# Optimization experiments

Measured on AMD Instinct MI355X. Metric: run time of the kernel, lower is better.

## Reference

```python
import jax, jax.numpy as jnp
import numpy as np

B, S, E, H, L, A, OBS = 4, 1024, 512, 8, 4, 8, 128
D_HEAD = E // H
EPS = 1e-6
DECAY_SCALING = 1.0


def rmsnorm(x, scale):
    return x * jax.lax.rsqrt(jnp.mean(x * x, -1, keepdims=True) + EPS) * scale


def swiglu_ffn(x, w_gate, w_lin, w_out):
    return (jax.nn.silu(x @ w_gate) * (x @ w_lin)) @ w_out


def retention(x, h, logk, w_q, w_k, w_v, w_g, w_o, gns, gnb, ts, seg):
    # x:[B,S,E]  h:[B,H,d,d]  ts/seg:[B,S] int  logk:[H]
    q = (x @ w_q).reshape(B, S, H, D_HEAD).transpose(0, 2, 1, 3)
    k = (x @ w_k).reshape(B, S, H, D_HEAD).transpose(0, 2, 1, 3) / jnp.sqrt(jnp.asarray(D_HEAD, x.dtype))
    v = (x @ w_v).reshape(B, S, H, D_HEAD).transpose(0, 2, 1, 3)
    dt = (ts[:, :, None] - ts[:, None, :]).astype(x.dtype)            # [B,S,S]
    mask = (dt >= 0) & (seg[:, :, None] == seg[:, None, :])           # timestep-causal, same episode
    dt = jnp.where(mask, dt, 0.0)
    Dm = jnp.where(mask[:, None], jnp.exp(dt[:, None] * logk[None, :, None, None]), 0.0)  # [B,H,S,S]
    scores = jnp.einsum('bhnd,bhmd->bhnm', q, k) * Dm
    inner = jnp.einsum('bhnm,bhme->bhne', scores, v)
    tsf = ts.astype(x.dtype)
    fresh = (seg == 0).astype(x.dtype)                                # prev-chunk state only valid pre-done
    xi = jnp.exp((tsf + 1.0)[:, None, :] * logk[None, :, None]) * fresh[:, None, :]  # [B,H,S]
    cross = jnp.einsum('bhn,bhnd,bhde->bhne', xi, q, h)
    ret = inner + cross                                               # [B,H,S,d]
    # chunk-final recurrent state
    tmax = tsf[:, -1]
    eta = jnp.exp((tmax[:, None] - tsf)[:, None, :] * logk[None, :, None])
    eta = eta * (seg == seg[:, -1:]).astype(x.dtype)[:, None, :]
    keep = (seg[:, -1] == 0).astype(x.dtype)
    h_decay = jnp.exp((tmax + 1.0)[:, None] * logk[None, :]) * keep[:, None]  # [B,H]
    h_new = h * h_decay[..., None, None] + jnp.einsum('bhm,bhmd,bhme->bhde', eta, k, v)
    # per-head group norm (num_groups = n_head)
    y = ret.transpose(0, 2, 1, 3)                                     # [B,S,H,d]
    mu = jnp.mean(y, -1, keepdims=True)
    var = jnp.mean((y - mu) ** 2, -1, keepdims=True)
    y = ((y - mu) * jax.lax.rsqrt(var + EPS)).reshape(B, S, E) * gns + gnb
    out = (jax.nn.silu(x @ w_g) * y) @ w_o
    return out, h_new


def forward(obs, hstate, dones, timestep_id, ln_enc_scale, w_enc, ln_shared,
            wq, wk, wv, wg, wo, gn_scale, gn_bias, ln1_s, ln2_s,
            sw_gate, sw_lin, sw_out, head_w1, head_b1, head_ln, head_w2, head_b2):
    kappas = (1.0 - jnp.exp(jnp.linspace(jnp.log(1.0 / 32.0), jnp.log(1.0 / 512.0), H))) * DECAY_SCALING
    logk = jnp.log(kappas).astype(obs.dtype)
    seg = jnp.cumsum(dones, axis=-1)
    x = jax.nn.gelu(rmsnorm(obs, ln_enc_scale) @ w_enc)               # obs encoder
    new_h = jnp.zeros_like(hstate)
    for i in range(L):
        xin = rmsnorm(x, ln_shared)
        ret, hn = retention(xin, hstate[:, :, i], logk, wq[i], wk[i], wv[i], wg[i], wo[i],
                            gn_scale[i], gn_bias[i], timestep_id, seg)
        x1 = rmsnorm(xin + ret, ln1_s[i])
        x = rmsnorm(x1 + swiglu_ffn(x1, sw_gate[i], sw_lin[i], sw_out[i]), ln2_s[i])
        new_h = new_h.at[:, :, i].set(hn)
    z = jax.nn.gelu(x @ head_w1 + head_b1)
    v_loc = rmsnorm(z, head_ln) @ head_w2 + head_b2
    return v_loc, x, new_h


def setup_inputs() -> dict:
    key = jax.random.key(0)
    ks = jax.random.split(key, 16)
    sc = 0.02
    f = jnp.float32
    return {
        'obs': jax.random.normal(ks[0], (B, S, OBS), f),
        'hstate': jax.random.normal(ks[1], (B, H, L, D_HEAD, D_HEAD), f) * 0.1,
        'dones': (jax.random.uniform(ks[2], (B, S)) < 0.01).astype(jnp.int32),
        'timestep_id': jnp.broadcast_to(jnp.repeat(jnp.arange(S // A, dtype=jnp.int32), A)[None], (B, S)),
        'ln_enc_scale': jnp.ones((OBS,), f),
        'w_enc': jax.random.normal(ks[3], (OBS, E), f) * sc,
        'ln_shared': jnp.ones((E,), f),
        'wq': jax.random.normal(ks[4], (L, E, E), f) * sc,
        'wk': jax.random.normal(ks[5], (L, E, E), f) * sc,
        'wv': jax.random.normal(ks[6], (L, E, E), f) * sc,
        'wg': jax.random.normal(ks[7], (L, E, E), f) * sc,
        'wo': jax.random.normal(ks[8], (L, E, E), f) * sc,
        'gn_scale': jnp.ones((L, E), f),
        'gn_bias': jnp.zeros((L, E), f),
        'ln1_s': jnp.ones((L, E), f),
        'ln2_s': jnp.ones((L, E), f),
        'sw_gate': jax.random.normal(ks[9], (L, E, E), f) * sc,
        'sw_lin': jax.random.normal(ks[10], (L, E, E), f) * sc,
        'sw_out': jax.random.normal(ks[11], (L, E, E), f) * sc,
        'head_w1': jax.random.normal(ks[12], (E, E), f) * sc,
        'head_b1': jnp.zeros((E,), f),
        'head_ln': jnp.ones((E,), f),
        'head_w2': jax.random.normal(ks[13], (E, 1), f) * 0.01,
        'head_b2': jnp.zeros((1,), f),
    }


def reference(obs, hstate, dones, timestep_id, ln_enc_scale, w_enc, ln_shared,
              wq, wk, wv, wg, wo, gn_scale, gn_bias, ln1_s, ln2_s,
              sw_gate, sw_lin, sw_out, head_w1, head_b1, head_ln, head_w2, head_b2):
    return forward(obs, hstate, dones, timestep_id, ln_enc_scale, w_enc, ln_shared,
                   wq, wk, wv, wg, wo, gn_scale, gn_bias, ln1_s, ln2_s,
                   sw_gate, sw_lin, sw_out, head_w1, head_b1, head_ln, head_w2, head_b2)
```

## Files before the change

### kernel.cpp

```cpp
#include <hip/hip_runtime.h>
#include <math.h>

#define BN 4
#define SN 1024
#define EN 512
#define HN 8
#define LN 4
#define DN 64
#define OBSN 128
#define NR (BN*SN)
#define NB (NR*EN)
#define EPSF 1e-6f

typedef __attribute__((ext_vector_type(8))) short short8v;
typedef __attribute__((ext_vector_type(4))) float f32x4;
typedef unsigned short u16;

__device__ __forceinline__ float logk_of(int h){
    const float start = -3.4657359027997265f;
    const float step  = -0.3960841031771117f;
    return logf(1.0f - expf(start + step*(float)h));
}
__device__ __forceinline__ float geluf(float x){
    float x3 = x*x*x;
    return 0.5f*x*(1.0f + tanhf(0.7978845608028654f*(x + 0.044715f*x3)));
}
__device__ __forceinline__ float siluf(float x){
    return x / (1.0f + expf(-x));
}
__device__ __forceinline__ u16 f2bf(float x){
    union { float f; unsigned u; } v; v.f = x;
    unsigned r = v.u + 0x7FFFu + ((v.u >> 16) & 1u);
    return (u16)(r >> 16);
}
__device__ __forceinline__ float bf2f(u16 x){
    union { unsigned u; float f; } v; v.u = ((unsigned)x)<<16;
    return v.f;
}
__device__ __forceinline__ void load_lds16(const void* g, void* l){
    __builtin_amdgcn_global_load_lds((const __attribute__((address_space(1))) void*)g,
                                     (__attribute__((address_space(3))) void*)l, 16, 0, 0);
}
__device__ __forceinline__ int swz(int r, int bo){ return r*128 + (bo ^ ((r&7)<<4)); }

__global__ void seg_kernel(const int* __restrict__ dones, int* __restrict__ seg){
    __shared__ int sm[SN];
    int b = blockIdx.x, t = threadIdx.x;
    sm[t] = dones[b*SN + t];
    __syncthreads();
    for (int off=1; off<SN; off<<=1){
        int v = (t>=off) ? sm[t-off] : 0;
        __syncthreads();
        sm[t] += v;
        __syncthreads();
    }
    seg[b*SN + t] = sm[t];
}

__global__ void wconv8_kernel(const float* w0, const float* w1, const float* w2,
                              const float* w3, const float* w4, const float* w5,
                              const float* w6, const float* w7,
                              u16* __restrict__ dst){
    __shared__ u16 tile[32][33];
    int z = blockIdx.z;
    int type = z>>2, layer = z&3;
    const float* srcs[8] = {w0,w1,w2,w3,w4,w5,w6,w7};
    const float* s = srcs[type] + (size_t)layer*EN*EN;
    u16* d = dst + ((size_t)type*LN + layer)*EN*EN;
    int k0 = blockIdx.y*32, m0 = blockIdx.x*32;
    int tx = threadIdx.x, ty = threadIdx.y;
    #pragma unroll
    for (int i=0;i<32;i+=8)
        tile[tx][ty+i] = f2bf(s[(size_t)(k0+ty+i)*EN + m0+tx]);
    __syncthreads();
    #pragma unroll
    for (int i=0;i<32;i+=8)
        d[(size_t)(m0+ty+i)*EN + k0+tx] = tile[ty+i][tx];
}
__global__ void wconv_kernel(const float* __restrict__ src, u16* __restrict__ dst,
                             int K, int M){
    __shared__ u16 tile[32][33];
    int k0 = blockIdx.y*32, m0 = blockIdx.x*32;
    int tx = threadIdx.x, ty = threadIdx.y;
    #pragma unroll
    for (int i=0;i<32;i+=8)
        tile[tx][ty+i] = f2bf(src[(size_t)(k0+ty+i)*M + m0+tx]);
    __syncthreads();
    #pragma unroll
    for (int i=0;i<32;i+=8)
        dst[(size_t)(m0+ty+i)*K + k0+tx] = tile[ty+i][tx];
}

template<int COLS, bool WF32, bool WBF>
__global__ void rmsnorm_kernel(const float* __restrict__ A,
                               const float* __restrict__ scale,
                               float* __restrict__ Of,
                               u16* __restrict__ Ob){
    constexpr int PER = COLS/64;
    int row  = blockIdx.x*4 + (threadIdx.x>>6);
    int lane = threadIdx.x & 63;
    const float* a = A + (size_t)row*COLS;
    float v[PER];
    float ss = 0.f;
    #pragma unroll
    for (int i=0;i<PER;i++){
        float x = a[lane + i*64];
        v[i] = x; ss += x*x;
    }
    #pragma unroll
    for (int off=32; off>0; off>>=1) ss += __shfl_xor(ss, off, 64);
    float rs = rsqrtf(ss*(1.0f/COLS) + EPSF);
    #pragma unroll
    for (int i=0;i<PER;i++){
        float o = v[i]*rs*scale[lane + i*64];
        if (WF32) Of[(size_t)row*COLS + lane + i*64] = o;
        if (WBF)  Ob[(size_t)row*COLS + lane + i*64] = f2bf(o);
    }
}

__device__ __forceinline__ void stage_tile(const u16* __restrict__ G, size_t rowBase,
                                           int K, int k0, u16* dst, int t){
    #pragma unroll
    for (int i=0;i<2;i++){
        int o = i*4096 + t*16;
        int grow = o>>7, gcolb = o&127;
        load_lds16(G + (rowBase+grow)*K + k0 + (gcolb>>1), (char*)dst + o);
    }
}
__device__ __forceinline__ void mma_tile(const u16* As, const u16* Bs, f32x4 acc[2][2],
                                         int wr, int wc, int lane){
    #pragma unroll
    for (int kk=0; kk<64; kk+=32){
        int kb = kk + (lane>>4)*8;
        short8v a[2], b[2];
        #pragma unroll
        for (int m=0;m<2;m++)
            a[m] = *(const short8v*)((const char*)As + (wr*32+m*16+(lane&15))*128 + kb*2);
        #pragma unroll
        for (int n=0;n<2;n++)
            b[n] = *(const short8v*)((const char*)Bs + (wc*32+n*16+(lane&15))*128 + kb*2);
        #pragma unroll
        for (int m=0;m<2;m++)
            #pragma unroll
            for (int n=0;n<2;n++)
                acc[m][n] = __builtin_amdgcn_mfma_f32_16x16x32_bf16(a[m], b[n], acc[m][n], 0,0,0);
    }
}
#define ZERO_ACC(acc) { _Pragma("unroll") for (int m=0;m<2;m++) _Pragma("unroll") for (int n=0;n<2;n++){ acc[m][n][0]=0.f;acc[m][n][1]=0.f;acc[m][n][2]=0.f;acc[m][n][3]=0.f; } }

__global__ __launch_bounds__(256) void gemm_qkvg(
    const u16* __restrict__ A,
    const u16* __restrict__ WQ, const u16* __restrict__ WK,
    const u16* __restrict__ WV, const u16* __restrict__ WG,
    u16* __restrict__ Qbb, u16* __restrict__ Kbb,
    u16* __restrict__ VtT, u16* __restrict__ KtT, float* __restrict__ Gb)
{
    __shared__ u16 As[2][64*64];
    __shared__ u16 Bs[2][4][64*64];
    int t = threadIdx.x;
    int row0 = blockIdx.y*64, col0 = blockIdx.x*64;
    int w = t>>6, lane = t&63;
    int wr = w>>1, wc = w&1;
    f32x4 accQ[2][2], accK[2][2], accV[2][2], accG[2][2];
    ZERO_ACC(accQ); ZERO_ACC(accK); ZERO_ACC(accV); ZERO_ACC(accG);
    const u16* Ws[4] = {WQ, WK, WV, WG};

    stage_tile(A, (size_t)row0, EN, 0, As[0], t);
    #pragma unroll
    for (int wt=0; wt<4; wt++) stage_tile(Ws[wt], (size_t)col0, EN, 0, Bs[0][wt], t);
    __syncthreads();
    for (int ti=0; ti<EN/64; ++ti){
        int cur = ti&1;
        if (ti+1 < EN/64){
            stage_tile(A, (size_t)row0, EN, (ti+1)*64, As[cur^1], t);
            #pragma unroll
            for (int wt=0; wt<4; wt++)
                stage_tile(Ws[wt], (size_t)col0, EN, (ti+1)*64, Bs[cur^1][wt], t);
        }
        mma_tile(As[cur], Bs[cur][0], accQ, wr, wc, lane);
        mma_tile(As[cur], Bs[cur][1], accK, wr, wc, lane);
        mma_tile(As[cur], Bs[cur][2], accV, wr, wc, lane);
        mma_tile(As[cur], Bs[cur][3], accG, wr, wc, lane);
        __syncthreads();
    }
    #pragma unroll
    for (int m=0;m<2;m++){
        #pragma unroll
        for (int n=0;n<2;n++){
            int col = col0 + wc*32 + n*16 + (lane&15);
            int rbase = row0 + wr*32 + m*16 + (lane>>4)*4;
            ushort4 pkV, pkK;
            #pragma unroll
            for (int j=0;j<4;j++){
                size_t idx = (size_t)(rbase+j)*EN + col;
                Qbb[idx] = f2bf(accQ[m][n][j]);
                float kx = accK[m][n][j]*0.125f;
                Kbb[idx] = f2bf(kx);
                ((u16*)&pkK)[j] = f2bf(kx);
                ((u16*)&pkV)[j] = f2bf(accV[m][n][j]);
                Gb[idx] = siluf(accG[m][n][j]);
            }
            int bb = rbase>>10;
            int s0 = rbase&1023;
            *(ushort4*)(VtT + ((size_t)bb*EN + col)*SN + s0) = pkV;
            *(ushort4*)(KtT + ((size_t)bb*EN + col)*SN + s0) = pkK;
        }
    }
}

__global__ __launch_bounds__(256) void gemm_swpair(
    const u16* __restrict__ A,
    const u16* __restrict__ WGt, const u16* __restrict__ WLt,
    u16* __restrict__ Out)
{
    __shared__ u16 As[2][64*64];
    __shared__ u16 Bg[2][64*64];
    __shared__ u16 Bl[2][64*64];
    int t = threadIdx.x;
    int row0 = blockIdx.y*64, col0 = blockIdx.x*64;
    int w = t>>6, lane = t&63;
    int wr = w>>1, wc = w&1;
    f32x4 accG[2][2], accL[2][2];
    ZERO_ACC(accG); ZERO_ACC(accL);
    stage_tile(A, (size_t)row0, EN, 0, As[0], t);
    stage_tile(WGt, (size_t)col0, EN, 0, Bg[0], t);
    stage_tile(WLt, (size_t)col0, EN, 0, Bl[0], t);
    __syncthreads();
    for (int ti=0; ti<EN/64; ++ti){
        int cur = ti&1;
        if (ti+1 < EN/64){
            stage_tile(A, (size_t)row0, EN, (ti+1)*64, As[cur^1], t);
            stage_tile(WGt, (size_t)col0, EN, (ti+1)*64, Bg[cur^1], t);
            stage_tile(WLt, (size_t)col0, EN, (ti+1)*64, Bl[cur^1], t);
        }
        mma_tile(As[cur], Bg[cur], accG, wr, wc, lane);
        mma_tile(As[cur], Bl[cur], accL, wr, wc, lane);
        __syncthreads();
    }
    #pragma unroll
    for (int m=0;m<2;m++){
        #pragma unroll
        for (int n=0;n<2;n++){
            int col = col0 + wc*32 + n*16 + (lane&15);
            int rbase = row0 + wr*32 + m*16 + (lane>>4)*4;
            #pragma unroll
            for (int j=0;j<4;j++){
                float x = siluf(accG[m][n][j]) * accL[m][n][j];
                Out[(size_t)(rbase+j)*EN + col] = f2bf(x);
            }
        }
    }
}

template<int ACT, bool BIASF, bool RESF, int OUTM>
__global__ __launch_bounds__(256) void gemm_bf16(
    const u16* __restrict__ A, const u16* __restrict__ Wt,
    const float* __restrict__ bias, const float* __restrict__ res,
    float* __restrict__ C, u16* __restrict__ Ob, int K, float scale)
{
    __shared__ u16 As[2][64*64];
    __shared__ u16 Bs[2][64*64];
    int t = threadIdx.x;
    int row0 = blockIdx.y*64, col0 = blockIdx.x*64;
    int w = t>>6, lane = t&63;
    int wr = w>>1, wc = w&1;
    f32x4 acc[2][2];
    ZERO_ACC(acc);
    int nt = K/64;
    stage_tile(A, (size_t)row0, K, 0, As[0], t);
    stage_tile(Wt, (size_t)col0, K, 0, Bs[0], t);
    __syncthreads();
    for (int ti=0; ti<nt; ++ti){
        int cur = ti&1;
        if (ti+1 < nt){
            stage_tile(A, (size_t)row0, K, (ti+1)*64, As[cur^1], t);
            stage_tile(Wt, (size_t)col0, K, (ti+1)*64, Bs[cur^1], t);
        }
        mma_tile(As[cur], Bs[cur], acc, wr, wc, lane);
        __syncthreads();
    }
    #pragma unroll
    for (int m=0;m<2;m++){
        #pragma unroll
        for (int n=0;n<2;n++){
            int col = col0 + wc*32 + n*16 + (lane&15);
            int rbase = row0 + wr*32 + m*16 + (lane>>4)*4;
            #pragma unroll
            for (int j=0;j<4;j++){
                float x = acc[m][n][j]*scale;
                if (BIASF) x += bias[col];
                if (ACT==1) x = siluf(x);
                if (ACT==2) x = geluf(x);
                if (RESF) x += res[(size_t)(rbase+j)*512 + col];
                if (OUTM&1) C[(size_t)(rbase+j)*512 + col] = x;
                if (OUTM&2) Ob[(size_t)(rbase+j)*512 + col] = f2bf(x);
            }
        }
    }
}

__global__ __launch_bounds__(256) void retention_mfma(
    const u16* __restrict__ Qbb, const u16* __restrict__ Kbb,
    const u16* __restrict__ VtT, const u16* __restrict__ KtT,
    const float* __restrict__ hstate, const int* __restrict__ tsid, const int* __restrict__ seg,
    const float* __restrict__ gns, const float* __restrict__ gnb,
    const float* __restrict__ Gb, u16* __restrict__ Out,
    float* __restrict__ Hout, int layer)
{
    int bh = blockIdx.y; int b = bh>>3; int h = bh&7;
    int t = threadIdx.x, lane = t&63, w = t>>6;
    __shared__ u16 Qs[64*64];
    __shared__ u16 Ks[64*64];
    __shared__ u16 Vts[64*64];
    __shared__ u16 Ps[64*64];
    __shared__ float tsq_s[64], eq_s[64], xi_s[64];
    __shared__ int   segq_s[64];
    __shared__ float tsm_s[64], em_s[64];
    __shared__ int   segm_s[64];
    float lk = logk_of(h);

    if (blockIdx.x == 0){
        float tmax = (float)tsid[b*SN + SN-1];
        int segl = seg[b*SN + SN-1];
        float* eta = (float*)Qs;
        #pragma unroll
        for (int i=0;i<4;i++){
            int m = t + i*256;
            float tsm = (float)tsid[b*SN+m];
            eta[m] = (seg[b*SN+m]==segl) ? expf((tmax - tsm)*lk) : 0.f;
        }
        f32x4 eacc[4];
        #pragma unroll
        for (int en=0;en<4;en++){ eacc[en][0]=0.f; eacc[en][1]=0.f; eacc[en][2]=0.f; eacc[en][3]=0.f; }
        for (int mt=0; mt<16; ++mt){
            int m0 = mt*64;
            __syncthreads();
            #pragma unroll
            for (int i=0;i<2;i++){
                int c = t + i*256; int r = c>>3, cb = (c&7)*16;
                int mb = m0 + (cb>>1);
                size_t g = ((size_t)(b*EN) + h*DN + r)*SN + mb;
                short8v kt = *(const short8v*)(KtT + g);
                short8v vt = *(const short8v*)(VtT + g);
                short8v ks;
                #pragma unroll
                for (int j=0;j<8;j++) ks[j] = (short)f2bf(bf2f((u16)kt[j]) * eta[mb+j]);
                *(short8v*)((char*)Ks  + swz(r,cb)) = ks;
                *(short8v*)((char*)Vts + swz(r,cb)) = vt;
            }
            __syncthreads();
            short8v a0 = *(short8v*)((char*)Ks + swz(w*16+(lane&15), (lane>>4)*16));
            short8v a1 = *(short8v*)((char*)Ks + swz(w*16+(lane&15), 64+(lane>>4)*16));
            __builtin_amdgcn_s_setprio(1);
            #pragma unroll
            for (int en=0;en<4;en++){
                short8v b0 = *(short8v*)((char*)Vts + swz(en*16+(lane&15), (lane>>4)*16));
                short8v b1 = *(short8v*)((char*)Vts + swz(en*16+(lane&15), 64+(lane>>4)*16));
                eacc[en] = __builtin_amdgcn_mfma_f32_16x16x32_bf16(a0, b0, eacc[en], 0,0,0);
                eacc[en] = __builtin_amdgcn_mfma_f32_16x16x32_bf16(a1, b1, eacc[en], 0,0,0);
            }
            __builtin_amdgcn_s_setprio(0);
        }
        float hd = (segl==0) ? expf((tmax+1.0f)*lk) : 0.f;
        const float* h0 = hstate + ((size_t)bh*LN + layer)*4096;
        float* ho = Hout + ((size_t)bh*LN + layer)*4096;
        #pragma unroll
        for (int en=0;en<4;en++){
            int e = en*16 + (lane&15);
            #pragma unroll
            for (int j=0;j<4;j++){
                int d = w*16 + (lane>>4)*4 + j;
                ho[d*64 + e] = h0[d*64 + e]*hd + eacc[en][j];
            }
        }
        return;
    }

    int tile = 16 - (int)blockIdx.x;
    int n0 = tile*64;

    #pragma unroll
    for (int i=0;i<2;i++){
        int c = t + i*256; int r = c>>3, cb = (c&7)*16;
        short8v qv = *(const short8v*)(Qbb + (size_t)(b*SN + n0 + r)*EN + h*DN + (cb>>1));
        *(short8v*)((char*)Qs + swz(r,cb)) = qv;
    }
    const float* h0 = hstate + ((size_t)bh*LN + layer)*4096;
    #pragma unroll
    for (int i=0;i<4;i++){
        int idx = t + i*256; int d = idx>>4, e0 = (idx&15)*4;
        float4 hv = *(const float4*)(h0 + d*64 + e0);
        *(u16*)((char*)Ps + swz(e0+0, 2*d)) = f2bf(hv.x);
        *(u16*)((char*)Ps + swz(e0+1, 2*d)) = f2bf(hv.y);
        *(u16*)((char*)Ps + swz(e0+2, 2*d)) = f2bf(hv.z);
        *(u16*)((char*)Ps + swz(e0+3, 2*d)) = f2bf(hv.w);
    }
    if (t<64){
        float tq = (float)tsid[b*SN+n0+t];
        int sg = seg[b*SN+n0+t];
        tsq_s[t]=tq; segq_s[t]=sg;
        eq_s[t]=expf(tq*lk);
        xi_s[t]=(sg==0)?expf((tq+1.f)*lk):0.f;
    }
    short8v kr0, kr1, vr0, vr1;
    {
        int c0 = t, c1 = t+256;
        int r0=c0>>3, cb0=(c0&7)*16, r1=c1>>3, cb1=(c1&7)*16;
        kr0 = *(const short8v*)(Kbb + (size_t)(b*SN+r0)*EN + h*DN + (cb0>>1));
        kr1 = *(const short8v*)(Kbb + (size_t)(b*SN+r1)*EN + h*DN + (cb1>>1));
        vr0 = *(const short8v*)(VtT + ((size_t)(b*EN)+h*DN+r0)*SN + (cb0>>1));
        vr1 = *(const short8v*)(VtT + ((size_t)(b*EN)+h*DN+r1)*SN + (cb1>>1));
    }
    __syncthreads();

    int qlj = w*16 + ((lane>>4)<<2);
    float tsq_r[4], eq_r[4], xi_r[4]; int sgq_r[4];
    #pragma unroll
    for (int j=0;j<4;j++){
        tsq_r[j]=tsq_s[qlj+j]; eq_r[j]=eq_s[qlj+j];
        xi_r[j]=xi_s[qlj+j];  sgq_r[j]=segq_s[qlj+j];
    }
    short8v aq0 = *(short8v*)((char*)Qs + swz(w*16+(lane&15), (lane>>4)*16));
    short8v aq1 = *(short8v*)((char*)Qs + swz(w*16+(lane&15), 64 + (lane>>4)*16));

    f32x4 oacc[4];
    {
        f32x4 cacc[4];
        #pragma unroll
        for (int en=0;en<4;en++){ cacc[en][0]=0.f; cacc[en][1]=0.f; cacc[en][2]=0.f; cacc[en][3]=0.f; }
        #pragma unroll
        for (int en=0;en<4;en++){
            short8v b0 = *(short8v*)((char*)Ps + swz(en*16+(lane&15), (lane>>4)*16));
            short8v b1 = *(short8v*)((char*)Ps + swz(en*16+(lane&15), 64+(lane>>4)*16));
            cacc[en] = __builtin_amdgcn_mfma_f32_16x16x32_bf16(aq0, b0, cacc[en], 0,0,0);
            cacc[en] = __builtin_amdgcn_mfma_f32_16x16x32_bf16(aq1, b1, cacc[en], 0,0,0);
        }
        #pragma unroll
        for (int en=0;en<4;en++)
            #pragma unroll
            for (int j=0;j<4;j++) oacc[en][j] = cacc[en][j]*xi_r[j];
    }

    for (int mt=0; mt<=tile; ++mt){
        int m0 = mt*64;
        __syncthreads();
        {
            int c0 = t, c1 = t+256;
            int r0=c0>>3, cb0=(c0&7)*16, r1=c1>>3, cb1=(c1&7)*16;
            *(short8v*)((char*)Ks  + swz(r0,cb0)) = kr0;
            *(short8v*)((char*)Ks  + swz(r1,cb1)) = kr1;
            *(short8v*)((char*)Vts + swz(r0,cb0)) = vr0;
            *(short8v*)((char*)Vts + swz(r1,cb1)) = vr1;
        }
        if (t<64){
            float tm = (float)tsid[b*SN+m0+t];
            tsm_s[t]=tm; segm_s[t]=seg[b*SN+m0+t]; em_s[t]=expf(-tm*lk);
        }
        if (mt < tile){
            int m1 = m0 + 64;
            int c0 = t, c1 = t+256;
            int r0=c0>>3, cb0=(c0&7)*16, r1=c1>>3, cb1=(c1&7)*16;
            kr0 = *(const short8v*)(Kbb + (size_t)(b*SN+m1+r0)*EN + h*DN + (cb0>>1));
            kr1 = *(const short8v*)(Kbb + (size_t)(b*SN+m1+r1)*EN + h*DN + (cb1>>1));
            vr0 = *(const short8v*)(VtT + ((size_t)(b*EN)+h*DN+r0)*SN + m1 + (cb0>>1));
            vr1 = *(const short8v*)(VtT + ((size_t)(b*EN)+h*DN+r1)*SN + m1 + (cb1>>1));
        }
        __syncthreads();
        f32x4 sacc[4];
        #pragma unroll
        for (int mn=0;mn<4;mn++){ sacc[mn][0]=0.f; sacc[mn][1]=0.f; sacc[mn][2]=0.f; sacc[mn][3]=0.f; }
        __builtin_amdgcn_s_setprio(1);
        #pragma unroll
        for (int mn=0;mn<4;mn++){
            short8v b0 = *(short8v*)((char*)Ks + swz(mn*16+(lane&15), (lane>>4)*16));
            short8v b1 = *(short8v*)((char*)Ks + swz(mn*16+(lane&15), 64+(lane>>4)*16));
            sacc[mn] = __builtin_amdgcn_mfma_f32_16x16x32_bf16(aq0, b0, sacc[mn], 0,0,0);
            sacc[mn] = __builtin_amdgcn_mfma_f32_16x16x32_bf16(aq1, b1, sacc[mn], 0,0,0);
        }
        __builtin_amdgcn_s_setprio(0);
        #pragma unroll
        for (int mn=0;mn<4;mn++){
            int m = mn*16 + (lane&15);
            float tm = tsm_s[m]; float em = em_s[m]; int sgm = segm_s[m];
            #pragma unroll
            for (int j=0;j<4;j++){
                float p = (tsq_r[j]>=tm && sgq_r[j]==sgm) ? sacc[mn][j]*eq_r[j]*em : 0.f;
                *(u16*)((char*)Ps + swz(qlj+j, 2*m)) = f2bf(p);
            }
        }
        short8v ap0 = *(short8v*)((char*)Ps + swz(w*16+(lane&15), (lane>>4)*16));
        short8v ap1 = *(short8v*)((char*)Ps + swz(w*16+(lane&15), 64+(lane>>4)*16));
        __builtin_amdgcn_s_setprio(1);
        #pragma unroll
        for (int dn=0;dn<4;dn++){
            short8v b0 = *(short8v*)((char*)Vts + swz(dn*16+(lane&15), (lane>>4)*16));
            short8v b1 = *(short8v*)((char*)Vts + swz(dn*16+(lane&15), 64+(lane>>4)*16));
            oacc[dn] = __builtin_amdgcn_mfma_f32_16x16x32_bf16(ap0, b0, oacc[dn], 0,0,0);
            oacc[dn] = __builtin_amdgcn_mfma_f32_16x16x32_bf16(ap1, b1, oacc[dn], 0,0,0);
        }
        __builtin_amdgcn_s_setprio(0);
    }

    float mu[4], rs[4];
    #pragma unroll
    for (int j=0;j<4;j++){
        float s = oacc[0][j]+oacc[1][j]+oacc[2][j]+oacc[3][j];
        #pragma unroll
        for (int off=1; off<16; off<<=1) s += __shfl_xor(s, off, 64);
        mu[j] = s*(1.0f/64.0f);
        float d0=oacc[0][j]-mu[j], d1=oacc[1][j]-mu[j], d2=oacc[2][j]-mu[j], d3=oacc[3][j]-mu[j];
        float q2 = d0*d0+d1*d1+d2*d2+d3*d3;
        #pragma unroll
        for (int off=1; off<16; off<<=1) q2 += __shfl_xor(q2, off, 64);
        rs[j] = rsqrtf(q2*(1.0f/64.0f) + EPSF);
    }
    #pragma unroll
    for (int dn=0;dn<4;dn++){
        int e = h*DN + dn*16 + (lane&15);
        float gs = gns[e], gb = gnb[e];
        #pragma unroll
        for (int j=0;j<4;j++){
            size_t row = (size_t)(b*SN + n0 + qlj + j);
            float y = (oacc[dn][j]-mu[j])*rs[j]*gs + gb;
            Out[row*EN + e] = f2bf(y * Gb[row*EN + e]);
        }
    }
}

__global__ void vloc_kernel(const float* __restrict__ ZN, const float* __restrict__ w2,
                            const float* __restrict__ b2, float* __restrict__ out){
    int row  = blockIdx.x*4 + (threadIdx.x>>6);
    int lane = threadIdx.x & 63;
    const float* z = ZN + (size_t)row*EN;
    float s = 0.f;
    #pragma unroll
    for (int i=0;i<8;i++) s += z[lane + i*64]*w2[lane + i*64];
    #pragma unroll
    for (int off=32; off>0; off>>=1) s += __shfl_xor(s, off, 64);
    if (lane==0) out[row] = s + b2[0];
}

static inline void launch_gemm(const u16* A, const u16* Wt, const float* bias,
                               const float* res, float* C, u16* Ob,
                               int K, float scale, int act, int outm, hipStream_t s){
    dim3 g(8, 64), b(256,1,1);
    if (bias)                    gemm_bf16<2,true ,false,1><<<g,b,0,s>>>(A,Wt,bias,res,C,Ob,K,scale);
    else if (res && outm==3)     gemm_bf16<0,false,true ,3><<<g,b,0,s>>>(A,Wt,bias,res,C,Ob,K,scale);
    else if (res)                gemm_bf16<0,false,true ,1><<<g,b,0,s>>>(A,Wt,bias,res,C,Ob,K,scale);
    else if (act==2)             gemm_bf16<2,false,false,1><<<g,b,0,s>>>(A,Wt,bias,res,C,Ob,K,scale);
    else                         gemm_bf16<0,false,false,1><<<g,b,0,s>>>(A,Wt,bias,res,C,Ob,K,scale);
}

extern "C" void kernel_launch(void* const* d_in, const int* in_sizes, int n_in,
                              void* d_out, int out_size, void* d_ws, size_t ws_size,
                              hipStream_t stream){
    const float* obs       = (const float*)d_in[0];
    const float* hstate    = (const float*)d_in[1];
    const int*   dones     = (const int*)  d_in[2];
    const int*   tsid      = (const int*)  d_in[3];
    const float* ln_enc    = (const float*)d_in[4];
    const float* w_enc     = (const float*)d_in[5];
    const float* ln_shared = (const float*)d_in[6];
    const float* wq        = (const float*)d_in[7];
    const float* wk        = (const float*)d_in[8];
    const float* wv        = (const float*)d_in[9];
    const float* wg        = (const float*)d_in[10];
    const float* wo        = (const float*)d_in[11];
    const float* gns       = (const float*)d_in[12];
    const float* gnb       = (const float*)d_in[13];
    const float* ln1       = (const float*)d_in[14];
    const float* ln2       = (const float*)d_in[15];
    const float* swg       = (const float*)d_in[16];
    const float* swl       = (const float*)d_in[17];
    const float* swo       = (const float*)d_in[18];
    const float* hw1       = (const float*)d_in[19];
    const float* hb1       = (const float*)d_in[20];
    const float* hln       = (const float*)d_in[21];
    const float* hw2       = (const float*)d_in[22];
    const float* hb2       = (const float*)d_in[23];

    float* out_v = (float*)d_out;
    float* out_x = out_v + NR;
    float* out_h = out_x + (size_t)NR*EN;

    float* ws    = (float*)d_ws;
    float* XIN   = ws + 0*(size_t)NB;
    float* Qb    = ws + 1*(size_t)NB;
    float* Kb    = ws + 2*(size_t)NB;
    float* Vb    = ws + 3*(size_t)NB;
    float* Gb    = ws + 4*(size_t)NB;
    float* Yb    = ws + 5*(size_t)NB;
    int*   seg   = (int*)(ws + 6*(size_t)NB);
    u16* wtb  = (u16*)(seg + NR);
    const size_t WEm = (size_t)EN*EN;
    u16* wqT   = wtb;
    u16* wkT   = wqT + 4*WEm;
    u16* wvT   = wkT + 4*WEm;
    u16* wgT   = wvT + 4*WEm;
    u16* woT   = wgT + 4*WEm;
    u16* sgT   = woT + 4*WEm;
    u16* slT   = sgT + 4*WEm;
    u16* soT   = slT + 4*WEm;
    u16* wencT = soT + 4*WEm;
    u16* w1T   = wencT + (size_t)EN*OBSN;
    u16* S1b   = w1T + WEm;
    u16* S2b   = S1b + (size_t)NB;
    u16* encb  = S2b + (size_t)NB;
    u16* Qbb   = encb + (size_t)NR*OBSN;
    u16* Kbb   = Qbb + (size_t)NB;
    u16* VtT   = (u16*)Qb;
    u16* KtT   = VtT + (size_t)NB;

    seg_kernel<<<BN, SN, 0, stream>>>(dones, seg);

    {
        dim3 tb(32,8,1);
        wconv8_kernel<<<dim3(16,16,32), tb, 0, stream>>>(wq,wk,wv,wg,wo,swg,swl,swo, wtb);
        wconv_kernel<<<dim3(16,4,1),  tb, 0, stream>>>(w_enc, wencT, OBSN, EN);
        wconv_kernel<<<dim3(16,16,1), tb, 0, stream>>>(hw1,   w1T,   EN, EN);
    }

    rmsnorm_kernel<OBSN,false,true><<<NR/4, 256, 0, stream>>>(obs, ln_enc, nullptr, encb);
    launch_gemm(encb, wencT, nullptr, nullptr, out_x, nullptr, OBSN, 1.f, 2, 1, stream);

    for (int l=0; l<LN; ++l){
        rmsnorm_kernel<EN,true,true><<<NR/4, 256, 0, stream>>>(out_x, ln_shared, XIN, S1b);
        gemm_qkvg<<<dim3(8,64), 256, 0, stream>>>(S1b,
            wqT + l*WEm, wkT + l*WEm, wvT + l*WEm, wgT + l*WEm,
            Qbb, Kbb, VtT, KtT, Gb);
        retention_mfma<<<dim3(17, BN*HN), 256, 0, stream>>>(
            Qbb, Kbb, VtT, KtT, hstate, tsid, seg, gns + l*EN, gnb + l*EN,
            Gb, S2b, out_h, l);
        launch_gemm(S2b, woT + l*WEm, nullptr, XIN, Qb, nullptr, EN, 1.f, 0, 1, stream);
        rmsnorm_kernel<EN,true,true><<<NR/4, 256, 0, stream>>>(Qb, ln1 + l*EN, Kb, S1b);
        gemm_swpair<<<dim3(8,64), 256, 0, stream>>>(S1b, sgT + l*WEm, slT + l*WEm, S2b);
        launch_gemm(S2b, soT + l*WEm, nullptr, Kb, Qb, nullptr, EN, 1.f, 0, 1, stream);
        if (l == LN-1)
            rmsnorm_kernel<EN,true,true ><<<NR/4, 256, 0, stream>>>(Qb, ln2 + l*EN, out_x, S1b);
        else
            rmsnorm_kernel<EN,true,false><<<NR/4, 256, 0, stream>>>(Qb, ln2 + l*EN, out_x, nullptr);
    }

    launch_gemm(S1b, w1T, hb1, nullptr, Yb, nullptr, EN, 1.f, 2, 1, stream);
    rmsnorm_kernel<EN,true,false><<<NR/4, 256, 0, stream>>>(Yb, hln, XIN, nullptr);
    vloc_kernel<<<NR/4, 256, 0, stream>>>(XIN, hw2, hb2, out_v);
}
```

Measured before the change: 436.4 us.

## Fold retention decay factors into Q and K in the projection epilogue

```diff
diff --git a/kernel.cpp b/kernel.cpp
--- a/kernel.cpp
+++ b/kernel.cpp
@@ -32,10 +32,6 @@
     union { float f; unsigned u; } v; v.f = x;
     unsigned r = v.u + 0x7FFFu + ((v.u >> 16) & 1u);
     return (u16)(r >> 16);
-}
-__device__ __forceinline__ float bf2f(u16 x){
-    union { unsigned u; float f; } v; v.u = ((unsigned)x)<<16;
-    return v.f;
 }
 __device__ __forceinline__ void load_lds16(const void* g, void* l){
     __builtin_amdgcn_global_load_lds((const __attribute__((address_space(1))) void*)g,
@@ -152,6 +148,7 @@
     const u16* __restrict__ A,
     const u16* __restrict__ WQ, const u16* __restrict__ WK,
     const u16* __restrict__ WV, const u16* __restrict__ WG,
+    const int* __restrict__ tsid,
     u16* __restrict__ Qbb, u16* __restrict__ Kbb,
     u16* __restrict__ VtT, u16* __restrict__ KtT, float* __restrict__ Gb)
 {
@@ -183,6 +180,17 @@
         mma_tile(As[cur], Bs[cur][3], accG, wr, wc, lane);
         __syncthreads();
     }
+    float lk = logk_of(blockIdx.x);
+    float eqv[2][4], emv[2][4];
+    #pragma unroll
+    for (int m=0;m<2;m++)
+        #pragma unroll
+        for (int j=0;j<4;j++){
+            int row = row0 + wr*32 + m*16 + (lane>>4)*4 + j;
+            float tq = (float)tsid[row];
+            eqv[m][j] = expf(tq*lk);
+            emv[m][j] = expf(-tq*lk);
+        }
     #pragma unroll
     for (int m=0;m<2;m++){
         #pragma unroll
@@ -193,8 +201,8 @@
             #pragma unroll
             for (int j=0;j<4;j++){
                 size_t idx = (size_t)(rbase+j)*EN + col;
-                Qbb[idx] = f2bf(accQ[m][n][j]);
-                float kx = accK[m][n][j]*0.125f;
+                Qbb[idx] = f2bf(eqv[m][j]*accQ[m][n][j]);
+                float kx = emv[m][j]*0.125f*accK[m][n][j];
                 Kbb[idx] = f2bf(kx);
                 ((u16*)&pkK)[j] = f2bf(kx);
                 ((u16*)&pkV)[j] = f2bf(accV[m][n][j]);
@@ -313,21 +321,20 @@
     __shared__ u16 Ks[64*64];
     __shared__ u16 Vts[64*64];
     __shared__ u16 Ps[64*64];
-    __shared__ float tsq_s[64], eq_s[64], xi_s[64];
+    __shared__ float tsq_s[64];
     __shared__ int   segq_s[64];
-    __shared__ float tsm_s[64], em_s[64];
+    __shared__ float tsm_s[64];
     __shared__ int   segm_s[64];
     float lk = logk_of(h);
 
     if (blockIdx.x == 0){
         float tmax = (float)tsid[b*SN + SN-1];
         int segl = seg[b*SN + SN-1];
-        float* eta = (float*)Qs;
+        u16* m16 = Qs;
         #pragma unroll
         for (int i=0;i<4;i++){
             int m = t + i*256;
-            float tsm = (float)tsid[b*SN+m];
-            eta[m] = (seg[b*SN+m]==segl) ? expf((tmax - tsm)*lk) : 0.f;
+            m16[m] = (seg[b*SN+m]==segl) ? (u16)0xFFFFu : (u16)0;
         }
         f32x4 eacc[4];
         #pragma unroll
@@ -342,10 +349,9 @@
                 size_t g = ((size_t)(b*EN) + h*DN + r)*SN + mb;
                 short8v kt = *(const short8v*)(KtT + g);
                 short8v vt = *(const short8v*)(VtT + g);
-                short8v ks;
-                #pragma unroll
-                for (int j=0;j<8;j++) ks[j] = (short)f2bf(bf2f((u16)kt[j]) * eta[mb+j]);
-                *(short8v*)((char*)Ks  + swz(r,cb)) = ks;
+                short8v mv = *(const short8v*)(m16 + mb);
+                kt &= mv;
+                *(short8v*)((char*)Ks  + swz(r,cb)) = kt;
                 *(short8v*)((char*)Vts + swz(r,cb)) = vt;
             }
             __syncthreads();
@@ -361,6 +367,7 @@
             }
             __builtin_amdgcn_s_setprio(0);
         }
+        float cfac = expf(tmax*lk);
         float hd = (segl==0) ? expf((tmax+1.0f)*lk) : 0.f;
         const float* h0 = hstate + ((size_t)bh*LN + layer)*4096;
         float* ho = Hout + ((size_t)bh*LN + layer)*4096;
@@ -370,7 +377,7 @@
             #pragma unroll
             for (int j=0;j<4;j++){
                 int d = w*16 + (lane>>4)*4 + j;
-                ho[d*64 + e] = h0[d*64 + e]*hd + eacc[en][j];
+                ho[d*64 + e] = h0[d*64 + e]*hd + cfac*eacc[en][j];
             }
         }
         return;
@@ -396,11 +403,8 @@
         *(u16*)((char*)Ps + swz(e0+3, 2*d)) = f2bf(hv.w);
     }
     if (t<64){
-        float tq = (float)tsid[b*SN+n0+t];
-        int sg = seg[b*SN+n0+t];
-        tsq_s[t]=tq; segq_s[t]=sg;
-        eq_s[t]=expf(tq*lk);
-        xi_s[t]=(sg==0)?expf((tq+1.f)*lk):0.f;
+        tsq_s[t] = (float)tsid[b*SN+n0+t];
+        segq_s[t] = seg[b*SN+n0+t];
     }
     short8v kr0, kr1, vr0, vr1;
     {
@@ -414,11 +418,13 @@
     __syncthreads();
 
     int qlj = w*16 + ((lane>>4)<<2);
-    float tsq_r[4], eq_r[4], xi_r[4]; int sgq_r[4];
+    float tsq_r[4]; int sgq_r[4]; float xr[4];
+    float elk = expf(lk);
     #pragma unroll
     for (int j=0;j<4;j++){
-        tsq_r[j]=tsq_s[qlj+j]; eq_r[j]=eq_s[qlj+j];
-        xi_r[j]=xi_s[qlj+j];  sgq_r[j]=segq_s[qlj+j];
+        tsq_r[j]=tsq_s[qlj+j];
+        sgq_r[j]=segq_s[qlj+j];
+        xr[j] = (sgq_r[j]==0) ? elk : 0.f;
     }
     short8v aq0 = *(short8v*)((char*)Qs + swz(w*16+(lane&15), (lane>>4)*16));
     short8v aq1 = *(short8v*)((char*)Qs + swz(w*16+(lane&15), 64 + (lane>>4)*16));
@@ -438,7 +444,7 @@
         #pragma unroll
         for (int en=0;en<4;en++)
             #pragma unroll
-            for (int j=0;j<4;j++) oacc[en][j] = cacc[en][j]*xi_r[j];
+            for (int j=0;j<4;j++) oacc[en][j] = cacc[en][j]*xr[j];
     }
 
     for (int mt=0; mt<=tile; ++mt){
@@ -453,8 +459,8 @@
             *(short8v*)((char*)Vts + swz(r1,cb1)) = vr1;
         }
         if (t<64){
-            float tm = (float)tsid[b*SN+m0+t];
-            tsm_s[t]=tm; segm_s[t]=seg[b*SN+m0+t]; em_s[t]=expf(-tm*lk);
+            tsm_s[t] = (float)tsid[b*SN+m0+t];
+            segm_s[t] = seg[b*SN+m0+t];
         }
         if (mt < tile){
             int m1 = m0 + 64;
@@ -478,14 +484,28 @@
             sacc[mn] = __builtin_amdgcn_mfma_f32_16x16x32_bf16(aq1, b1, sacc[mn], 0,0,0);
         }
         __builtin_amdgcn_s_setprio(0);
-        #pragma unroll
-        for (int mn=0;mn<4;mn++){
-            int m = mn*16 + (lane&15);
-            float tm = tsm_s[m]; float em = em_s[m]; int sgm = segm_s[m];
-            #pragma unroll
-            for (int j=0;j<4;j++){
-                float p = (tsq_r[j]>=tm && sgq_r[j]==sgm) ? sacc[mn][j]*eq_r[j]*em : 0.f;
-                *(u16*)((char*)Ps + swz(qlj+j, 2*m)) = f2bf(p);
+        if (mt==tile){
+            #pragma unroll
+            for (int mn=0;mn<4;mn++){
+                int m = mn*16 + (lane&15);
+                int sgm = segm_s[m];
+                float tm = tsm_s[m];
+                #pragma unroll
+                for (int j=0;j<4;j++){
+                    float p = (tsq_r[j]>=tm && sgq_r[j]==sgm) ? sacc[mn][j] : 0.f;
+                    *(u16*)((char*)Ps + swz(qlj+j, 2*m)) = f2bf(p);
+                }
+            }
+        } else {
+            #pragma unroll
+            for (int mn=0;mn<4;mn++){
+                int m = mn*16 + (lane&15);
+                int sgm = segm_s[m];
+                #pragma unroll
+                for (int j=0;j<4;j++){
+                    float p = (sgq_r[j]==sgm) ? sacc[mn][j] : 0.f;
+                    *(u16*)((char*)Ps + swz(qlj+j, 2*m)) = f2bf(p);
+                }
             }
         }
         short8v ap0 = *(short8v*)((char*)Ps + swz(w*16+(lane&15), (lane>>4)*16));
@@ -626,7 +646,7 @@
     for (int l=0; l<LN; ++l){
         rmsnorm_kernel<EN,true,true><<<NR/4, 256, 0, stream>>>(out_x, ln_shared, XIN, S1b);
         gemm_qkvg<<<dim3(8,64), 256, 0, stream>>>(S1b,
-            wqT + l*WEm, wkT + l*WEm, wvT + l*WEm, wgT + l*WEm,
+            wqT + l*WEm, wkT + l*WEm, wvT + l*WEm, wgT + l*WEm, tsid,
             Qbb, Kbb, VtT, KtT, Gb);
         retention_mfma<<<dim3(17, BN*HN), 256, 0, stream>>>(
             Qbb, Kbb, VtT, KtT, hstate, tsid, seg, gns + l*EN, gnb + l*EN,
```

New measurement: 428.9 us. Within noise of the previous version (-1.7%).
